# Optimization experiments

Measured on AMD Instinct MI355X. Metric: run time of the kernel, lower is better.

Reference implementation:

```python
import jax, jax.numpy as jnp
import numpy as np
from jax import lax

EPS = 1e-8
ROOT_2 = 1.41421
STYLE_SIZE = 512
OUT_CH = 512
STYLE_SCALE = (2.0 / STYLE_SIZE) ** 0.5   # Weight_Scaling(style_size): equalized-LR sqrt(2/fan_in)
OUT_SCALE = (2.0 / (OUT_CH * 1 * 1)) ** 0.5  # Weight_Scaling(out_channels*1*1)


def setup_inputs() -> dict:
    key = jax.random.key(0)
    ks = jax.random.split(key, 10)
    B, Cin, Cout, H, S = 8, 512, 512, 32, 512
    return {
        "x": jax.random.normal(ks[0], (B, Cin, H, H), dtype=jnp.float32),
        "style_base": jax.random.normal(ks[1], (B, S), dtype=jnp.float32),
        "noise": jax.random.normal(ks[2], (B, 1, 2 * H, 2 * H), dtype=jnp.float32),
        "t": jax.random.normal(ks[3], (B, Cout, 2 * H, 2 * H), dtype=jnp.float32),
        # learned params
        "affine_w": jax.random.normal(ks[4], (Cin, S), dtype=jnp.float32) * (1.0 / np.sqrt(S)),
        "affine_b": jnp.zeros((Cin,), dtype=jnp.float32),
        "conv_w": jax.random.normal(ks[5], (Cout, Cin, 3, 3), dtype=jnp.float32),
        "conv_b": jnp.zeros((1, Cout, 1, 1), dtype=jnp.float32),
        "prelu_a": jnp.asarray(0.25, dtype=jnp.float32),
        "noise_scalar": jnp.zeros((1, Cout, 1, 1), dtype=jnp.float32) + 0.1,
        "out_w": jax.random.normal(ks[6], (3, Cout, 1, 1), dtype=jnp.float32) * (1.0 / np.sqrt(Cout)),
        "out_b": jnp.zeros((3,), dtype=jnp.float32),
    }


def reference(x, style_base, noise, t, affine_w, affine_b, conv_w, conv_b,
              prelu_a, noise_scalar, out_w, out_b):
    B, Cin, H, W = x.shape
    # style_std = affine(Weight_Scaling(style_base)) + 1  -> [B, Cin]
    style_std = (style_base * STYLE_SCALE) @ affine_w.T + affine_b + 1.0

    # bilinear x2 upsample (align_corners=False == half-pixel, matches jax.image.resize)
    x = jax.image.resize(x, (B, Cin, 2 * H, 2 * W), method="bilinear")

    # modulated conv with L2 demodulation, expressed as input-scale + conv + output-scale
    # per-sample weight w_b[o,i,k,l] = w[o,i,k,l]*s[b,i] / ||w*s||_b,o
    wsq = jnp.sum(conv_w ** 2, axis=(2, 3))                      # [O, I]
    demod = 1.0 / jnp.sqrt(jnp.einsum("oi,bi->bo", wsq, style_std ** 2) + EPS)  # [B, O]
    xm = x * style_std[:, :, None, None]
    y = lax.conv_general_dilated(xm, conv_w, (1, 1), "SAME",
                                 dimension_numbers=("NCHW", "OIHW", "NCHW"))
    y = y * demod[:, :, None, None] + conv_b + noise_scalar * noise
    # PReLU (single shared slope)
    y = jnp.where(y >= 0, y, prelu_a * y)

    # out branch: skip add, scale, toRGB 1x1 conv, clamp
    y = (y + t) / ROOT_2
    out = lax.conv_general_dilated(y * OUT_SCALE, out_w, (1, 1), "SAME",
                                   dimension_numbers=("NCHW", "OIHW", "NCHW"))
    out = jnp.clip(out + out_b[None, :, None, None], 0.0, 1.0)
    return (y, out)
```

## Files before the change

### kernel.cpp

```cpp
#include <hip/hip_runtime.h>


typedef short bf16x8 __attribute__((ext_vector_type(8)));
typedef short short8v __attribute__((ext_vector_type(8)));
typedef float f32x16 __attribute__((ext_vector_type(16)));

#define WS_STYLE 0
#define WS_DEMOD 16384
#define WS_WSQ   32768
#define WS_WPACK 1081344
#define WS_XM    5799936

__device__ __forceinline__ short f2bf(float f) {
  unsigned u = __float_as_uint(f);
  u += 0x7FFFu + ((u >> 16) & 1u);
  return (short)(u >> 16);
}

__device__ __forceinline__ void gld16(const short* g, char* l) {
  __builtin_amdgcn_global_load_lds((const __attribute__((address_space(1))) void*)g,
                                   (__attribute__((address_space(3))) void*)l,
                                   16, 0, 0);
}

__global__ void k_style(const float* __restrict__ sb, const float* __restrict__ aw,
                        const float* __restrict__ ab, float* __restrict__ style) {
  __shared__ float s_sb[512];
  int b = blockIdx.x;
  for (int i = threadIdx.x; i < 512; i += 256) s_sb[i] = sb[b * 512 + i] * 0.0625f;
  __syncthreads();
  for (int i = threadIdx.x; i < 512; i += 256) {
    const float4* wrow = (const float4*)(aw + (size_t)i * 512);
    float acc = 0.f;
    #pragma unroll 4
    for (int s4 = 0; s4 < 128; ++s4) {
      float4 w4 = wrow[s4];
      float4 sv = *(const float4*)(s_sb + s4 * 4);
      acc += w4.x * sv.x + w4.y * sv.y + w4.z * sv.z + w4.w * sv.w;
    }
    style[b * 512 + i] = acc + ab[i] + 1.0f;
  }
}

__global__ void k_wsq(const float* __restrict__ cw, float* __restrict__ wsq) {
  int idx = blockIdx.x * 256 + threadIdx.x;
  const float* p = cw + (size_t)idx * 9;
  float s = 0.f;
  #pragma unroll
  for (int j = 0; j < 9; ++j) s += p[j] * p[j];
  wsq[idx] = s;
}

__global__ void k_demod(const float* __restrict__ wsq, const float* __restrict__ style,
                        float* __restrict__ demod) {
  int wid = threadIdx.x >> 6, lane = threadIdx.x & 63;
  int idx = blockIdx.x * 4 + wid;
  int b = idx >> 9, o = idx & 511;
  const float* wr = wsq + (size_t)o * 512;
  const float* ss = style + b * 512;
  float sum = 0.f;
  #pragma unroll
  for (int k = 0; k < 8; ++k) {
    int i = k * 64 + lane;
    float s = ss[i];
    sum += wr[i] * s * s;
  }
  #pragma unroll
  for (int off = 32; off; off >>= 1) sum += __shfl_down(sum, off);
  if (lane == 0) demod[b * 512 + o] = rsqrtf(sum + 1e-8f);
}

__global__ void k_upsample(const float* __restrict__ x, const float* __restrict__ style,
                           short* __restrict__ xm) {
  int b = blockIdx.x / 66, hp = blockIdx.x % 66;
  short* xmp = xm + ((size_t)b * 66 + hp) * 66 * 512;
  if (hp == 0 || hp == 65) {
    short8v z = {0, 0, 0, 0, 0, 0, 0, 0};
    for (int u = threadIdx.x; u < 66 * 512 / 8; u += 256) ((short8v*)xmp)[u] = z;
    return;
  }
  int h = hp - 1;
  int j0 = (h >> 1) - 1 + (h & 1);
  float fj = (h & 1) ? 0.25f : 0.75f;
  int j0c = j0 < 0 ? 0 : j0;
  int j1c = j0 + 1 > 31 ? 31 : j0 + 1;
  __shared__ float xt[2][64][33];
  int ccc = threadIdx.x & 63;
  int wsub = threadIdx.x >> 6;
  for (int c0 = 0; c0 < 512; c0 += 64) {
    __syncthreads();
    #pragma unroll 4
    for (int k = 0; k < 16; ++k) {
      int idx = k * 256 + threadIdx.x;
      int ii = idx & 31, cc = (idx >> 5) & 63, jj = idx >> 11;
      xt[jj][cc][ii] = x[(((size_t)b * 512 + c0 + cc) * 32 + (jj ? j1c : j0c)) * 32 + ii];
    }
    __syncthreads();
    float sstyle = style[b * 512 + c0 + ccc];
    #pragma unroll 4
    for (int wk = 0; wk < 16; ++wk) {
      int w = wk * 4 + wsub;
      int i0 = (w >> 1) - 1 + (w & 1);
      float fi = (w & 1) ? 0.25f : 0.75f;
      int i0c = i0 < 0 ? 0 : i0;
      int i1c = i0 + 1 > 31 ? 31 : i0 + 1;
      float v0 = xt[0][ccc][i0c] * (1.f - fi) + xt[0][ccc][i1c] * fi;
      float v1 = xt[1][ccc][i0c] * (1.f - fi) + xt[1][ccc][i1c] * fi;
      float v = (v0 * (1.f - fj) + v1 * fj) * sstyle;
      xmp[(size_t)(w + 1) * 512 + c0 + ccc] = f2bf(v);
    }
    if (wsub == 0) {
      xmp[c0 + ccc] = 0;
      xmp[(size_t)65 * 512 + c0 + ccc] = 0;
    }
  }
}

__global__ void k_packw(const float* __restrict__ cw, short* __restrict__ wpk) {
  int unit = blockIdx.x * 256 + threadIdx.x;
  int s = unit >> 11;
  int rem = unit & 2047;
  int o = rem >> 2, sp = rem & 3;
  int tap = s >> 4, cc = s & 15;
  int i0 = cc * 32 + ((sp ^ ((o >> 1) & 3)) << 3);
  const float* src = cw + ((size_t)o * 512 + i0) * 9 + tap;
  short8v v;
  #pragma unroll
  for (int j = 0; j < 8; ++j) v[j] = f2bf(src[j * 9]);
  *(short8v*)(wpk + (size_t)unit * 8) = v;
}

__global__ __launch_bounds__(256, 2) void k_conv(
    const short* __restrict__ xm, const short* __restrict__ wpk,
    const float* __restrict__ demod, const float* __restrict__ convb,
    const float* __restrict__ nscal, const float* __restrict__ noise,
    const float* __restrict__ t, const float* __restrict__ prelu_a,
    float* __restrict__ y) {
  __shared__ char XMs[2][16896];
  __shared__ char WTs[2][16384];

  int tid = threadIdx.x;
  int bid = blockIdx.x;
  int nt = bid & 1, hpair = (bid >> 1) & 31, b = bid >> 6;
  int wid = tid >> 6, lane = tid & 63;
  int wo = wid & 1, wsrow = wid >> 1;
  int l31 = lane & 31, lg = lane >> 5;

  const short* xb = xm + ((size_t)b * 66 + hpair * 2) * 66 * 512;
  int wb0 = ((wo * 128 + l31) << 6) + ((lg ^ ((l31 >> 1) & 3)) << 4);

  #pragma unroll
  for (int k = 0; k < 4; ++k) {
    int u = k * 256 + tid;
    int r = u / 264, rem = u - r * 264;
    int wp = rem >> 2, spp = rem & 3;
    gld16(xb + (size_t)(r * 66 + wp) * 512 + ((spp ^ ((wp >> 1) & 3)) << 3), XMs[0] + u * 16);
  }
  if (tid < 32) {
    int u = 1024 + tid;
    int rem = u - 792;
    int wp = rem >> 2, spp = rem & 3;
    gld16(xb + (size_t)(3 * 66 + wp) * 512 + ((spp ^ ((wp >> 1) & 3)) << 3), XMs[0] + u * 16);
  }
  #pragma unroll
  for (int k = 0; k < 4; ++k) {
    int u = k * 256 + tid;
    gld16(wpk + (size_t)(nt * 256) * 32 + u * 8, WTs[0] + u * 16);
  }

  f32x16 zf = {0,0,0,0,0,0,0,0,0,0,0,0,0,0,0,0};
  f32x16 acc[4][2];
  #pragma unroll
  for (int i = 0; i < 4; ++i) { acc[i][0] = zf; acc[i][1] = zf; }

  #pragma unroll 1
  for (int cc = 0; cc < 16; ++cc) {
    const char* XMc = XMs[cc & 1];
    char* XMn = XMs[(cc & 1) ^ 1];
    #pragma unroll
    for (int tap = 0; tap < 9; ++tap) {
      const int kh = tap / 3, kw = tap % 3;
      const char* WTc = WTs[(cc + tap) & 1];
      char* WTn = (char*)WTs[(cc + tap + 1) & 1];

      asm volatile("s_waitcnt vmcnt(0) lgkmcnt(0)" ::: "memory");
      __builtin_amdgcn_s_barrier();
      __builtin_amdgcn_sched_barrier(0);

      if (!(cc == 15 && tap == 8)) {
        int ntap = (tap < 8) ? (tap + 1) : 0;
        int ncc  = (tap < 8) ? cc : (cc + 1);
        const short* wsrc = wpk + ((size_t)((ntap * 16 + ncc) * 512) + nt * 256) * 32;
        #pragma unroll
        for (int k = 0; k < 4; ++k) {
          int u = k * 256 + tid;
          gld16(wsrc + u * 8, WTn + u * 16);
        }
      }
      if (tap <= 5 && cc < 15 && tid < 176) {
        int u = tap * 176 + tid;
        int r = u / 264, rem = u - r * 264;
        int wp = rem >> 2, spp = rem & 3;
        gld16(xb + (size_t)(r * 66 + wp) * 512 + (cc + 1) * 32 + ((spp ^ ((wp >> 1) & 3)) << 3),
              XMn + u * 16);
      }

      int a = l31 + kw;
      int xo = ((wsrow + kh) * 66 + a) * 64 + ((lg ^ ((a >> 1) & 3)) << 4);
      bf16x8 xf00 = *(const bf16x8*)(XMc + xo);
      bf16x8 xf01 = *(const bf16x8*)(XMc + xo + 2048);
      bf16x8 xf10 = *(const bf16x8*)(XMc + (xo ^ 32));
      bf16x8 xf11 = *(const bf16x8*)(XMc + ((xo ^ 32) + 2048));
      bf16x8 wf00 = *(const bf16x8*)(WTc + wb0);
      bf16x8 wf01 = *(const bf16x8*)(WTc + wb0 + 2048);
      bf16x8 wf02 = *(const bf16x8*)(WTc + wb0 + 4096);
      bf16x8 wf03 = *(const bf16x8*)(WTc + wb0 + 6144);
      bf16x8 wf10 = *(const bf16x8*)(WTc + (wb0 ^ 32));
      bf16x8 wf11 = *(const bf16x8*)(WTc + ((wb0 ^ 32) + 2048));
      bf16x8 wf12 = *(const bf16x8*)(WTc + ((wb0 ^ 32) + 4096));
      bf16x8 wf13 = *(const bf16x8*)(WTc + ((wb0 ^ 32) + 6144));

      __builtin_amdgcn_s_setprio(1);
      acc[0][0] = __builtin_amdgcn_mfma_f32_32x32x16_bf16(wf00, xf00, acc[0][0], 0, 0, 0);
      acc[0][1] = __builtin_amdgcn_mfma_f32_32x32x16_bf16(wf00, xf01, acc[0][1], 0, 0, 0);
      acc[1][0] = __builtin_amdgcn_mfma_f32_32x32x16_bf16(wf01, xf00, acc[1][0], 0, 0, 0);
      acc[1][1] = __builtin_amdgcn_mfma_f32_32x32x16_bf16(wf01, xf01, acc[1][1], 0, 0, 0);
      acc[2][0] = __builtin_amdgcn_mfma_f32_32x32x16_bf16(wf02, xf00, acc[2][0], 0, 0, 0);
      acc[2][1] = __builtin_amdgcn_mfma_f32_32x32x16_bf16(wf02, xf01, acc[2][1], 0, 0, 0);
      acc[3][0] = __builtin_amdgcn_mfma_f32_32x32x16_bf16(wf03, xf00, acc[3][0], 0, 0, 0);
      acc[3][1] = __builtin_amdgcn_mfma_f32_32x32x16_bf16(wf03, xf01, acc[3][1], 0, 0, 0);
      acc[0][0] = __builtin_amdgcn_mfma_f32_32x32x16_bf16(wf10, xf10, acc[0][0], 0, 0, 0);
      acc[0][1] = __builtin_amdgcn_mfma_f32_32x32x16_bf16(wf10, xf11, acc[0][1], 0, 0, 0);
      acc[1][0] = __builtin_amdgcn_mfma_f32_32x32x16_bf16(wf11, xf10, acc[1][0], 0, 0, 0);
      acc[1][1] = __builtin_amdgcn_mfma_f32_32x32x16_bf16(wf11, xf11, acc[1][1], 0, 0, 0);
      acc[2][0] = __builtin_amdgcn_mfma_f32_32x32x16_bf16(wf12, xf10, acc[2][0], 0, 0, 0);
      acc[2][1] = __builtin_amdgcn_mfma_f32_32x32x16_bf16(wf12, xf11, acc[2][1], 0, 0, 0);
      acc[3][0] = __builtin_amdgcn_mfma_f32_32x32x16_bf16(wf13, xf10, acc[3][0], 0, 0, 0);
      acc[3][1] = __builtin_amdgcn_mfma_f32_32x32x16_bf16(wf13, xf11, acc[3][1], 0, 0, 0);
      __builtin_amdgcn_s_setprio(0);
    }
  }

  float pa = prelu_a[0];
  const float inv_r2 = 1.0f / 1.41421f;
  int h = hpair * 2 + wsrow;
  float nz0 = noise[((size_t)b * 64 + h) * 64 + l31];
  float nz1 = noise[((size_t)b * 64 + h) * 64 + 32 + l31];
  #pragma unroll
  for (int cf = 0; cf < 4; ++cf) {
    #pragma unroll
    for (int reg = 0; reg < 16; ++reg) {
      int orow = (reg & 3) + 8 * (reg >> 2) + 4 * lg;
      int o = nt * 256 + wo * 128 + cf * 32 + orow;
      float dm = demod[b * 512 + o];
      float cb = convb[o];
      float ns = nscal[o];
      #pragma unroll
      for (int nf = 0; nf < 2; ++nf) {
        int w = nf * 32 + l31;
        float v = acc[cf][nf][reg];
        v = v * dm + cb + ns * (nf ? nz1 : nz0);
        v = (v >= 0.f) ? v : pa * v;
        size_t oi = (((size_t)b * 512 + o) * 64 + h) * 64 + w;
        v = (v + t[oi]) * inv_r2;
        y[oi] = v;
      }
    }
  }
}

__global__ void k_rgb(const float* __restrict__ y, const float* __restrict__ ow,
                      const float* __restrict__ ob, float* __restrict__ out) {
  int b = blockIdx.x >> 6, h = blockIdx.x & 63;
  int w = threadIdx.x & 63, g = threadIdx.x >> 6;
  const float* yb = y + (((size_t)b * 512) * 64 + h) * 64 + w;
  float s0 = 0.f, s1 = 0.f, s2 = 0.f;
  for (int o = g * 128; o < g * 128 + 128; ++o) {
    float v = yb[(size_t)o * 4096];
    s0 += v * ow[o];
    s1 += v * ow[512 + o];
    s2 += v * ow[1024 + o];
  }
  __shared__ float red[3][4][64];
  red[0][g][w] = s0; red[1][g][w] = s1; red[2][g][w] = s2;
  __syncthreads();
  if (threadIdx.x < 192) {
    int c = threadIdx.x >> 6, ww = threadIdx.x & 63;
    float s = red[c][0][ww] + red[c][1][ww] + red[c][2][ww] + red[c][3][ww];
    s = s * 0.0625f + ob[c];
    s = fminf(fmaxf(s, 0.f), 1.f);
    out[(((size_t)b * 3 + c) * 64 + h) * 64 + ww] = s;
  }
}

extern "C" void kernel_launch(void* const* d_in, const int* in_sizes, int n_in,
                              void* d_out, int out_size, void* d_ws, size_t ws_size,
                              hipStream_t stream) {
  const float* x     = (const float*)d_in[0];
  const float* sb    = (const float*)d_in[1];
  const float* noise = (const float*)d_in[2];
  const float* t     = (const float*)d_in[3];
  const float* aw    = (const float*)d_in[4];
  const float* ab    = (const float*)d_in[5];
  const float* cw    = (const float*)d_in[6];
  const float* cb    = (const float*)d_in[7];
  const float* pa    = (const float*)d_in[8];
  const float* ns    = (const float*)d_in[9];
  const float* ow    = (const float*)d_in[10];
  const float* ob    = (const float*)d_in[11];
  char* ws = (char*)d_ws;
  float* style = (float*)(ws + WS_STYLE);
  float* demod = (float*)(ws + WS_DEMOD);
  float* wsq   = (float*)(ws + WS_WSQ);
  short* wpk   = (short*)(ws + WS_WPACK);
  short* xm    = (short*)(ws + WS_XM);
  float* y   = (float*)d_out;
  float* out = y + 16777216;

  k_style<<<8, 256, 0, stream>>>(sb, aw, ab, style);
  k_wsq<<<1024, 256, 0, stream>>>(cw, wsq);
  k_demod<<<1024, 256, 0, stream>>>(wsq, style, demod);
  k_upsample<<<528, 256, 0, stream>>>(x, style, xm);
  k_packw<<<1152, 256, 0, stream>>>(cw, wpk);
  k_conv<<<512, 256, 0, stream>>>(xm, wpk, demod, cb, ns, noise, t, pa, y);
  k_rgb<<<512, 256, 0, stream>>>(y, ow, ob, out);
}
```

Measured before the change: 259.4 us.

## Load conv weights directly into registers, bypassing LDS staging

Weight fragments for the MFMA are now read straight from global memory into registers, with one tap of prefetch, instead of being staged through double-buffered LDS. The weight pack drops its XOR swizzle to match the new direct access pattern. With weights out of LDS, the per-tap barrier is only needed once per input-channel chunk, where the activation buffer swaps. The cost is more global/L2 traffic, because each wave now fetches its own weight rows, plus more registers held for the prefetched fragments. Global load latency may also be exposed if a single tap of prefetch is not enough to cover it.

```diff
diff --git a/kernel.cpp b/kernel.cpp
--- a/kernel.cpp
+++ b/kernel.cpp
@@ -120,9 +120,9 @@
   int unit = blockIdx.x * 256 + threadIdx.x;
   int s = unit >> 11;
   int rem = unit & 2047;
-  int o = rem >> 2, sp = rem & 3;
+  int o = rem >> 2, kg = rem & 3;
   int tap = s >> 4, cc = s & 15;
-  int i0 = cc * 32 + ((sp ^ ((o >> 1) & 3)) << 3);
+  int i0 = cc * 32 + (kg << 3);
   const float* src = cw + ((size_t)o * 512 + i0) * 9 + tap;
   short8v v;
   #pragma unroll
@@ -137,7 +137,6 @@
     const float* __restrict__ t, const float* __restrict__ prelu_a,
     float* __restrict__ y) {
   __shared__ char XMs[2][16896];
-  __shared__ char WTs[2][16384];
 
   int tid = threadIdx.x;
   int bid = blockIdx.x;
@@ -147,7 +146,7 @@
   int l31 = lane & 31, lg = lane >> 5;
 
   const short* xb = xm + ((size_t)b * 66 + hpair * 2) * 66 * 512;
-  int wb0 = ((wo * 128 + l31) << 6) + ((lg ^ ((l31 >> 1) & 3)) << 4);
+  const short* wlp = wpk + (size_t)((nt * 256 + wo * 128 + l31) * 32 + lg * 8);
 
   #pragma unroll
   for (int k = 0; k < 4; ++k) {
@@ -162,16 +161,24 @@
     int wp = rem >> 2, spp = rem & 3;
     gld16(xb + (size_t)(3 * 66 + wp) * 512 + ((spp ^ ((wp >> 1) & 3)) << 3), XMs[0] + u * 16);
   }
-  #pragma unroll
-  for (int k = 0; k < 4; ++k) {
-    int u = k * 256 + tid;
-    gld16(wpk + (size_t)(nt * 256) * 32 + u * 8, WTs[0] + u * 16);
-  }
+
+  bf16x8 wc0 = *(const bf16x8*)(wlp + 0);
+  bf16x8 wc1 = *(const bf16x8*)(wlp + 1024);
+  bf16x8 wc2 = *(const bf16x8*)(wlp + 2048);
+  bf16x8 wc3 = *(const bf16x8*)(wlp + 3072);
+  bf16x8 wc4 = *(const bf16x8*)(wlp + 16);
+  bf16x8 wc5 = *(const bf16x8*)(wlp + 1040);
+  bf16x8 wc6 = *(const bf16x8*)(wlp + 2064);
+  bf16x8 wc7 = *(const bf16x8*)(wlp + 3088);
 
   f32x16 zf = {0,0,0,0,0,0,0,0,0,0,0,0,0,0,0,0};
   f32x16 acc[4][2];
   #pragma unroll
   for (int i = 0; i < 4; ++i) { acc[i][0] = zf; acc[i][1] = zf; }
+
+  asm volatile("s_waitcnt vmcnt(0) lgkmcnt(0)" ::: "memory");
+  __builtin_amdgcn_s_barrier();
+  __builtin_amdgcn_sched_barrier(0);
 
   #pragma unroll 1
   for (int cc = 0; cc < 16; ++cc) {
@@ -180,22 +187,20 @@
     #pragma unroll
     for (int tap = 0; tap < 9; ++tap) {
       const int kh = tap / 3, kw = tap % 3;
-      const char* WTc = WTs[(cc + tap) & 1];
-      char* WTn = (char*)WTs[(cc + tap + 1) & 1];
-
-      asm volatile("s_waitcnt vmcnt(0) lgkmcnt(0)" ::: "memory");
-      __builtin_amdgcn_s_barrier();
-      __builtin_amdgcn_sched_barrier(0);
-
-      if (!(cc == 15 && tap == 8)) {
+
+      bf16x8 wn0, wn1, wn2, wn3, wn4, wn5, wn6, wn7;
+      {
         int ntap = (tap < 8) ? (tap + 1) : 0;
-        int ncc  = (tap < 8) ? cc : (cc + 1);
-        const short* wsrc = wpk + ((size_t)((ntap * 16 + ncc) * 512) + nt * 256) * 32;
-        #pragma unroll
-        for (int k = 0; k < 4; ++k) {
-          int u = k * 256 + tid;
-          gld16(wsrc + u * 8, WTn + u * 16);
-        }
+        int ncc  = (tap < 8) ? cc : (cc + 1 < 16 ? cc + 1 : 15);
+        const short* wsrc = wlp + (size_t)(ntap * 16 + ncc) * 16384;
+        wn0 = *(const bf16x8*)(wsrc + 0);
+        wn1 = *(const bf16x8*)(wsrc + 1024);
+        wn2 = *(const bf16x8*)(wsrc + 2048);
+        wn3 = *(const bf16x8*)(wsrc + 3072);
+        wn4 = *(const bf16x8*)(wsrc + 16);
+        wn5 = *(const bf16x8*)(wsrc + 1040);
+        wn6 = *(const bf16x8*)(wsrc + 2064);
+        wn7 = *(const bf16x8*)(wsrc + 3088);
       }
       if (tap <= 5 && cc < 15 && tid < 176) {
         int u = tap * 176 + tid;
@@ -211,33 +216,34 @@
       bf16x8 xf01 = *(const bf16x8*)(XMc + xo + 2048);
       bf16x8 xf10 = *(const bf16x8*)(XMc + (xo ^ 32));
       bf16x8 xf11 = *(const bf16x8*)(XMc + ((xo ^ 32) + 2048));
-      bf16x8 wf00 = *(const bf16x8*)(WTc + wb0);
-      bf16x8 wf01 = *(const bf16x8*)(WTc + wb0 + 2048);
-      bf16x8 wf02 = *(const bf16x8*)(WTc + wb0 + 4096);
-      bf16x8 wf03 = *(const bf16x8*)(WTc + wb0 + 6144);
-      bf16x8 wf10 = *(const bf16x8*)(WTc + (wb0 ^ 32));
-      bf16x8 wf11 = *(const bf16x8*)(WTc + ((wb0 ^ 32) + 2048));
-      bf16x8 wf12 = *(const bf16x8*)(WTc + ((wb0 ^ 32) + 4096));
-      bf16x8 wf13 = *(const bf16x8*)(WTc + ((wb0 ^ 32) + 6144));
 
       __builtin_amdgcn_s_setprio(1);
-      acc[0][0] = __builtin_amdgcn_mfma_f32_32x32x16_bf16(wf00, xf00, acc[0][0], 0, 0, 0);
-      acc[0][1] = __builtin_amdgcn_mfma_f32_32x32x16_bf16(wf00, xf01, acc[0][1], 0, 0, 0);
-      acc[1][0] = __builtin_amdgcn_mfma_f32_32x32x16_bf16(wf01, xf00, acc[1][0], 0, 0, 0);
-      acc[1][1] = __builtin_amdgcn_mfma_f32_32x32x16_bf16(wf01, xf01, acc[1][1], 0, 0, 0);
-      acc[2][0] = __builtin_amdgcn_mfma_f32_32x32x16_bf16(wf02, xf00, acc[2][0], 0, 0, 0);
-      acc[2][1] = __builtin_amdgcn_mfma_f32_32x32x16_bf16(wf02, xf01, acc[2][1], 0, 0, 0);
-      acc[3][0] = __builtin_amdgcn_mfma_f32_32x32x16_bf16(wf03, xf00, acc[3][0], 0, 0, 0);
-      acc[3][1] = __builtin_amdgcn_mfma_f32_32x32x16_bf16(wf03, xf01, acc[3][1], 0, 0, 0);
-      acc[0][0] = __builtin_amdgcn_mfma_f32_32x32x16_bf16(wf10, xf10, acc[0][0], 0, 0, 0);
-      acc[0][1] = __builtin_amdgcn_mfma_f32_32x32x16_bf16(wf10, xf11, acc[0][1], 0, 0, 0);
-      acc[1][0] = __builtin_amdgcn_mfma_f32_32x32x16_bf16(wf11, xf10, acc[1][0], 0, 0, 0);
-      acc[1][1] = __builtin_amdgcn_mfma_f32_32x32x16_bf16(wf11, xf11, acc[1][1], 0, 0, 0);
-      acc[2][0] = __builtin_amdgcn_mfma_f32_32x32x16_bf16(wf12, xf10, acc[2][0], 0, 0, 0);
-      acc[2][1] = __builtin_amdgcn_mfma_f32_32x32x16_bf16(wf12, xf11, acc[2][1], 0, 0, 0);
-      acc[3][0] = __builtin_amdgcn_mfma_f32_32x32x16_bf16(wf13, xf10, acc[3][0], 0, 0, 0);
-      acc[3][1] = __builtin_amdgcn_mfma_f32_32x32x16_bf16(wf13, xf11, acc[3][1], 0, 0, 0);
+      acc[0][0] = __builtin_amdgcn_mfma_f32_32x32x16_bf16(wc0, xf00, acc[0][0], 0, 0, 0);
+      acc[0][1] = __builtin_amdgcn_mfma_f32_32x32x16_bf16(wc0, xf01, acc[0][1], 0, 0, 0);
+      acc[1][0] = __builtin_amdgcn_mfma_f32_32x32x16_bf16(wc1, xf00, acc[1][0], 0, 0, 0);
+      acc[1][1] = __builtin_amdgcn_mfma_f32_32x32x16_bf16(wc1, xf01, acc[1][1], 0, 0, 0);
+      acc[2][0] = __builtin_amdgcn_mfma_f32_32x32x16_bf16(wc2, xf00, acc[2][0], 0, 0, 0);
+      acc[2][1] = __builtin_amdgcn_mfma_f32_32x32x16_bf16(wc2, xf01, acc[2][1], 0, 0, 0);
+      acc[3][0] = __builtin_amdgcn_mfma_f32_32x32x16_bf16(wc3, xf00, acc[3][0], 0, 0, 0);
+      acc[3][1] = __builtin_amdgcn_mfma_f32_32x32x16_bf16(wc3, xf01, acc[3][1], 0, 0, 0);
+      acc[0][0] = __builtin_amdgcn_mfma_f32_32x32x16_bf16(wc4, xf10, acc[0][0], 0, 0, 0);
+      acc[0][1] = __builtin_amdgcn_mfma_f32_32x32x16_bf16(wc4, xf11, acc[0][1], 0, 0, 0);
+      acc[1][0] = __builtin_amdgcn_mfma_f32_32x32x16_bf16(wc5, xf10, acc[1][0], 0, 0, 0);
+      acc[1][1] = __builtin_amdgcn_mfma_f32_32x32x16_bf16(wc5, xf11, acc[1][1], 0, 0, 0);
+      acc[2][0] = __builtin_amdgcn_mfma_f32_32x32x16_bf16(wc6, xf10, acc[2][0], 0, 0, 0);
+      acc[2][1] = __builtin_amdgcn_mfma_f32_32x32x16_bf16(wc6, xf11, acc[2][1], 0, 0, 0);
+      acc[3][0] = __builtin_amdgcn_mfma_f32_32x32x16_bf16(wc7, xf10, acc[3][0], 0, 0, 0);
+      acc[3][1] = __builtin_amdgcn_mfma_f32_32x32x16_bf16(wc7, xf11, acc[3][1], 0, 0, 0);
       __builtin_amdgcn_s_setprio(0);
+
+      wc0 = wn0; wc1 = wn1; wc2 = wn2; wc3 = wn3;
+      wc4 = wn4; wc5 = wn5; wc6 = wn6; wc7 = wn7;
+
+      if (tap == 8) {
+        asm volatile("s_waitcnt vmcnt(0) lgkmcnt(0)" ::: "memory");
+        __builtin_amdgcn_s_barrier();
+        __builtin_amdgcn_sched_barrier(0);
+      }
     }
   }
 
```

Measured after the change: 254.6 us. No clear change (-1.9%).
